# Kernel tuning notes

Hardware: AMD Instinct MI355X
Metric: run time of the kernel (lower is better)

## Reference

```python
import jax, jax.numpy as jnp
import numpy as np

DIM = 1024
HEADS = 16
HEAD_DIM = DIM // HEADS
THRESH = 0.29514
SHARP = 15.0
LN_EPS = 1e-5
NORM_EPS = 1e-12


def setup_inputs() -> dict:
    key = jax.random.key(0)
    ks = jax.random.split(key, 8)
    s = 1.0 / np.sqrt(DIM)
    sg = 1.0 / np.sqrt(HEAD_DIM)
    return {
        "x": jax.random.normal(ks[0], (2, 2048, DIM), dtype=jnp.float32),
        "Wq": jax.random.uniform(ks[1], (DIM, DIM), jnp.float32, -s, s),
        "Wk": jax.random.uniform(ks[2], (DIM, DIM), jnp.float32, -s, s),
        "Wv": jax.random.uniform(ks[3], (DIM, DIM), jnp.float32, -s, s),
        "gq": jax.random.uniform(ks[4], (HEAD_DIM,), jnp.float32, -sg, sg),
        "gk": jax.random.uniform(ks[5], (HEAD_DIM,), jnp.float32, -sg, sg),
        "Wo": jax.random.uniform(ks[6], (DIM, DIM), jnp.float32, -s, s),
        "bo": jax.random.uniform(ks[7], (DIM,), jnp.float32, -s, s),
        "ln_w": jnp.ones((DIM,), jnp.float32),
        "ln_b": jnp.zeros((DIM,), jnp.float32),
    }


def _l2norm(t):
    # F.normalize: t / max(||t||_2, eps)
    n = jnp.sqrt(jnp.sum(t * t, axis=-1, keepdims=True))
    return t / jnp.maximum(n, NORM_EPS)


def reference(x, Wq, Wk, Wv, gq, gk, Wo, bo, ln_w, ln_b):
    B, T, D = x.shape
    # LayerNorm over last dim
    mu = jnp.mean(x, axis=-1, keepdims=True)
    var = jnp.mean((x - mu) ** 2, axis=-1, keepdims=True)
    x_norm = (x - mu) / jnp.sqrt(var + LN_EPS) * ln_w + ln_b

    def split_heads(t):  # [B,T,D] -> [B,H,T,hd]
        return t.reshape(B, T, HEADS, HEAD_DIM).transpose(0, 2, 1, 3)

    q = _l2norm(split_heads(x_norm @ Wq))
    k = _l2norm(split_heads(x_norm @ Wk))
    v = split_heads(x @ Wv)  # note: v uses un-normalized x, as in source

    align = jnp.einsum("bhtd,bhsd->bhts", q, k)  # cosine alignment
    resonance = jax.nn.sigmoid((align - THRESH) * SHARP)
    gate_q = jnp.einsum("bhtd,d->bht", q, gq)
    gate_k = jnp.einsum("bhsd,d->bhs", k, gk)
    modulation = resonance * gate_q[..., :, None] * gate_k[..., None, :]
    collapse = jnp.einsum("bhts,bhsd->bhtd", modulation, v)
    collapse = collapse.transpose(0, 2, 1, 3).reshape(B, T, D)
    return collapse @ Wo + bo
```

## Files before the change

### kernel.cpp

```cpp
#include <hip/hip_runtime.h>
#include <math.h>

#define DIM 1024
#define T_SEQ 2048
#define NBATCH 2
#define HEADS 16
#define HD 64
#define NTOK 4096
#define THRESH 0.29514f
#define SHARP 15.0f
#define LOG2E 1.4426950408889634f

typedef __attribute__((ext_vector_type(8))) short bf16x8;
typedef __attribute__((ext_vector_type(4))) float f32x4;

__device__ __forceinline__ unsigned short f2b(float f) {
    unsigned int u = __float_as_uint(f);
    unsigned int r = (u + 0x7FFFu + ((u >> 16) & 1u)) >> 16;
    return (unsigned short)r;
}
__device__ __forceinline__ float b2f(unsigned short u) {
    return __uint_as_float(((unsigned int)u) << 16);
}

__device__ __forceinline__ void async_cp16(const unsigned short* g, unsigned short* l) {
    __builtin_amdgcn_global_load_lds(
        (const __attribute__((address_space(1))) unsigned int*)g,
        (__attribute__((address_space(3))) unsigned int*)l, 16, 0, 0);
}

__global__ __launch_bounds__(256) void ln_xnorm_kernel(
    const float* __restrict__ x, const float* __restrict__ lnw, const float* __restrict__ lnb,
    unsigned short* __restrict__ xnb, unsigned short* __restrict__ xb) {
    int row = blockIdx.x * 4 + (threadIdx.x >> 6);
    int lane = threadIdx.x & 63;
    const float4* xr = (const float4*)(x + (size_t)row * DIM);
    float4 v[4];
    float s = 0.f, ss = 0.f;
#pragma unroll
    for (int i = 0; i < 4; i++) {
        v[i] = xr[lane + i * 64];
        s += v[i].x + v[i].y + v[i].z + v[i].w;
        ss += v[i].x * v[i].x + v[i].y * v[i].y + v[i].z * v[i].z + v[i].w * v[i].w;
    }
#pragma unroll
    for (int off = 32; off; off >>= 1) {
        s += __shfl_xor(s, off);
        ss += __shfl_xor(ss, off);
    }
    float m = s * (1.f / DIM);
    float rstd = rsqrtf(ss * (1.f / DIM) - m * m + 1e-5f);
#pragma unroll
    for (int i = 0; i < 4; i++) {
        int e = (lane + i * 64) * 4;
        float4 lw = *(const float4*)&lnw[e];
        float4 lb = *(const float4*)&lnb[e];
        ushort4 un, ur;
        un.x = f2b((v[i].x - m) * rstd * lw.x + lb.x);
        un.y = f2b((v[i].y - m) * rstd * lw.y + lb.y);
        un.z = f2b((v[i].z - m) * rstd * lw.z + lb.z);
        un.w = f2b((v[i].w - m) * rstd * lw.w + lb.w);
        ur.x = f2b(v[i].x); ur.y = f2b(v[i].y); ur.z = f2b(v[i].z); ur.w = f2b(v[i].w);
        *(ushort4*)&xnb[(size_t)row * DIM + e] = un;
        *(ushort4*)&xb[(size_t)row * DIM + e] = ur;
    }
}

__global__ __launch_bounds__(256) void wtrans_kernel(
    const float* __restrict__ W0, const float* __restrict__ W1,
    const float* __restrict__ W2, const float* __restrict__ W3,
    unsigned short* __restrict__ T0, unsigned short* __restrict__ T1,
    unsigned short* __restrict__ T2, unsigned short* __restrict__ T3) {
    __shared__ float tile[64][65];
    const int z = blockIdx.z;
    const float* W = (z == 0) ? W0 : (z == 1) ? W1 : (z == 2) ? W2 : W3;
    unsigned short* T = (z == 0) ? T0 : (z == 1) ? T1 : (z == 2) ? T2 : T3;
    const int k0 = blockIdx.x * 64, n0 = blockIdx.y * 64;
    const int r = threadIdx.x >> 3;
    const int c = (threadIdx.x & 7) * 8;
#pragma unroll
    for (int half = 0; half < 2; half++) {
        int rr = r + half * 32;
        float4 a = *(const float4*)&W[(size_t)(k0 + rr) * DIM + n0 + c];
        float4 b = *(const float4*)&W[(size_t)(k0 + rr) * DIM + n0 + c + 4];
        tile[rr][c + 0] = a.x; tile[rr][c + 1] = a.y; tile[rr][c + 2] = a.z; tile[rr][c + 3] = a.w;
        tile[rr][c + 4] = b.x; tile[rr][c + 5] = b.y; tile[rr][c + 6] = b.z; tile[rr][c + 7] = b.w;
    }
    __syncthreads();
#pragma unroll
    for (int half = 0; half < 2; half++) {
        int dd = r + half * 32;
        bf16x8 o;
#pragma unroll
        for (int j = 0; j < 8; j++) o[j] = (short)f2b(tile[c + j][dd]);
        *(bf16x8*)&T[(size_t)(n0 + dd) * DIM + k0 + c] = o;
    }
}

template <int MODE>
__global__ __launch_bounds__(256) void gemm_mfma_kernel(
    const unsigned short* __restrict__ A0, const unsigned short* __restrict__ A2,
    const unsigned short* __restrict__ Bt0, const unsigned short* __restrict__ Bt1,
    const unsigned short* __restrict__ Bt2, const float* __restrict__ bias,
    const float* __restrict__ gq, const float* __restrict__ gk,
    unsigned short* __restrict__ Oq, unsigned short* __restrict__ Ok,
    unsigned short* __restrict__ Ov, float* __restrict__ gq_t, float* __restrict__ gk_t,
    float* __restrict__ Oout) {
    __shared__ __align__(16) unsigned short As[128 * 32];
    __shared__ __align__(16) unsigned short Bs[128 * 32];
    const int tid = threadIdx.x;
    const int lane = tid & 63, w = tid >> 6;
    const int l16 = lane & 15, quad = lane >> 4;
    const int wm = w >> 1, wn = w & 1;
    const int m0 = blockIdx.x * 128, n0 = blockIdx.y * 128;
    const unsigned short* A;
    const unsigned short* Bt;
    int z = 0;
    if constexpr (MODE == 0) {
        z = blockIdx.z;
        A = (z == 2) ? A2 : A0;
        Bt = (z == 0) ? Bt0 : (z == 1) ? Bt1 : Bt2;
    } else {
        A = A0;
        Bt = Bt0;
    }
    f32x4 acc[4][4] = {};
    const int kswz = (l16 >> 1) & 3;

    for (int k0 = 0; k0 < DIM; k0 += 32) {
        __syncthreads();
#pragma unroll
        for (int i = 0; i < 2; i++) {
            int linear = i * 256 + tid;
            int m = linear >> 2, kgp = linear & 3;
            int kgl = kgp ^ ((m >> 1) & 3);
            async_cp16(A + (size_t)(m0 + m) * DIM + k0 + kgl * 8, As + linear * 8);
            async_cp16(Bt + (size_t)(n0 + m) * DIM + k0 + kgl * 8, Bs + linear * 8);
        }
        __syncthreads();
        bf16x8 af[4], bfr[4];
#pragma unroll
        for (int t = 0; t < 4; t++) {
            int ma = wm * 64 + t * 16 + l16;
            af[t] = *(const bf16x8*)(As + ma * 32 + ((quad ^ kswz) * 8));
            int nb = wn * 64 + t * 16 + l16;
            bfr[t] = *(const bf16x8*)(Bs + nb * 32 + ((quad ^ kswz) * 8));
        }
#pragma unroll
        for (int mt = 0; mt < 4; mt++)
#pragma unroll
            for (int nt = 0; nt < 4; nt++)
                acc[mt][nt] =
                    __builtin_amdgcn_mfma_f32_16x16x32_bf16(af[mt], bfr[nt], acc[mt][nt], 0, 0, 0);
    }

    if constexpr (MODE == 0) {
        const int h = (n0 + wn * 64) >> 6;
        if (z <= 1) {
            const float* gvec = (z == 0) ? gq : gk;
            float* gate = (z == 0) ? gq_t : gk_t;
            unsigned short* O = (z == 0) ? Oq : Ok;
            float gv[4];
#pragma unroll
            for (int nt = 0; nt < 4; nt++) gv[nt] = gvec[nt * 16 + l16];
#pragma unroll
            for (int mt = 0; mt < 4; mt++) {
#pragma unroll
                for (int r = 0; r < 4; r++) {
                    float ss = 0.f;
#pragma unroll
                    for (int nt = 0; nt < 4; nt++) ss += acc[mt][nt][r] * acc[mt][nt][r];
#pragma unroll
                    for (int msk = 1; msk < 16; msk <<= 1) ss += __shfl_xor(ss, msk);
                    float rn = __builtin_amdgcn_rcpf(fmaxf(sqrtf(ss), 1e-12f));
                    float vn[4], gg = 0.f;
#pragma unroll
                    for (int nt = 0; nt < 4; nt++) {
                        vn[nt] = acc[mt][nt][r] * rn;
                        gg += vn[nt] * gv[nt];
                    }
#pragma unroll
                    for (int msk = 1; msk < 16; msk <<= 1) gg += __shfl_xor(gg, msk);
                    int tok = m0 + wm * 64 + mt * 16 + quad * 4 + r;
                    int b = tok >> 11, t = tok & 2047;
                    size_t rowbase = ((size_t)(b * HEADS + h) * T_SEQ + t) * HD;
#pragma unroll
                    for (int nt = 0; nt < 4; nt++) O[rowbase + nt * 16 + l16] = f2b(vn[nt]);
                    if (l16 == 0) gate[(b * HEADS + h) * T_SEQ + t] = gg;
                }
            }
        } else {
#pragma unroll
            for (int mt = 0; mt < 4; mt++) {
#pragma unroll
                for (int r = 0; r < 4; r++) {
                    int tok = m0 + wm * 64 + mt * 16 + quad * 4 + r;
                    int b = tok >> 11, t = tok & 2047;
                    size_t rowbase = ((size_t)(b * HEADS + h) * T_SEQ + t) * HD;
#pragma unroll
                    for (int nt = 0; nt < 4; nt++)
                        Ov[rowbase + nt * 16 + l16] = f2b(acc[mt][nt][r]);
                }
            }
        }
    } else {
        float bias_r[4];
#pragma unroll
        for (int nt = 0; nt < 4; nt++) bias_r[nt] = bias[n0 + wn * 64 + nt * 16 + l16];
#pragma unroll
        for (int mt = 0; mt < 4; mt++) {
#pragma unroll
            for (int r = 0; r < 4; r++) {
                int tok = m0 + wm * 64 + mt * 16 + quad * 4 + r;
#pragma unroll
                for (int nt = 0; nt < 4; nt++) {
                    int n = n0 + wn * 64 + nt * 16 + l16;
                    Oout[(size_t)tok * DIM + n] = acc[mt][nt][r] + bias_r[nt];
                }
            }
        }
    }
}

__global__ __launch_bounds__(256) void vtrans_kernel(const unsigned short* __restrict__ Vn,
                                                     const float* __restrict__ gk_t,
                                                     unsigned short* __restrict__ Vt) {
    __shared__ float tile[64][65];
    const int bh = blockIdx.y;
    const int t0 = blockIdx.x * 64;
    const int r = threadIdx.x >> 3;
    const int c = (threadIdx.x & 7) * 8;
    const unsigned short* src = Vn + (size_t)bh * T_SEQ * HD;
#pragma unroll
    for (int half = 0; half < 2; half++) {
        int rr = r + half * 32;
        float gkv = gk_t[bh * T_SEQ + t0 + rr];
        bf16x8 v = *(const bf16x8*)(src + (size_t)(t0 + rr) * HD + c);
#pragma unroll
        for (int j = 0; j < 8; j++) tile[rr][c + j] = b2f((unsigned short)v[j]) * gkv;
    }
    __syncthreads();
    unsigned short* dst = Vt + (size_t)bh * HD * T_SEQ;
#pragma unroll
    for (int half = 0; half < 2; half++) {
        int dd = r + half * 32;
        bf16x8 o;
#pragma unroll
        for (int j = 0; j < 8; j++) o[j] = (short)f2b(tile[c + j][dd]);
        *(bf16x8*)(dst + (size_t)dd * T_SEQ + t0 + c) = o;
    }
}

__global__ __launch_bounds__(256) void attn_mfma_kernel(
    const unsigned short* __restrict__ Qn, const unsigned short* __restrict__ Kn,
    const unsigned short* __restrict__ Vt, const float* __restrict__ gateq,
    unsigned short* __restrict__ collb) {
    __shared__ __align__(16) unsigned short Ks[64 * 72];
    __shared__ __align__(16) unsigned short VtL[64 * 72];
    __shared__ __align__(16) unsigned short Sw[4 * 16 * 72];
    const int tid = threadIdx.x;
    const int lane = tid & 63, w = tid >> 6;
    const int quad = lane >> 4, l16 = lane & 15;
    const int t0 = blockIdx.x * 64;
    const int h = blockIdx.y, b = blockIdx.z;
    const int bh = b * HEADS + h;
    const size_t base = (size_t)bh * T_SEQ * HD;
    constexpr float K1 = -SHARP * LOG2E;
    constexpr float K0 = THRESH * SHARP * LOG2E;

    const unsigned short* qrow = Qn + base + (size_t)(t0 + w * 16 + l16) * HD;
    bf16x8 fq0 = *(const bf16x8*)(qrow + quad * 8);
    bf16x8 fq1 = *(const bf16x8*)(qrow + 32 + quad * 8);

    f32x4 oacc[4] = {};
    unsigned short* myS = &Sw[w * 16 * 72];
    const int sr = tid >> 3;
    const int sc = (tid & 7) * 8;

    for (int s0 = 0; s0 < T_SEQ; s0 += 64) {
        __syncthreads();
#pragma unroll
        for (int half = 0; half < 2; half++) {
            int rr = sr + half * 32;
            bf16x8 kv = *(const bf16x8*)(Kn + base + (size_t)(s0 + rr) * HD + sc);
            *(bf16x8*)(Ks + rr * 72 + sc) = kv;
            bf16x8 vv = *(const bf16x8*)(Vt + base + (size_t)rr * T_SEQ + s0 + sc);
            *(bf16x8*)(VtL + rr * 72 + sc) = vv;
        }
        __syncthreads();

#pragma unroll
        for (int ct = 0; ct < 4; ct++) {
            f32x4 sacc = {0.f, 0.f, 0.f, 0.f};
            bf16x8 fk0 = *(const bf16x8*)(Ks + (ct * 16 + l16) * 72 + quad * 8);
            bf16x8 fk1 = *(const bf16x8*)(Ks + (ct * 16 + l16) * 72 + 32 + quad * 8);
            sacc = __builtin_amdgcn_mfma_f32_16x16x32_bf16(fq0, fk0, sacc, 0, 0, 0);
            sacc = __builtin_amdgcn_mfma_f32_16x16x32_bf16(fq1, fk1, sacc, 0, 0, 0);
#pragma unroll
            for (int r = 0; r < 4; r++) {
                float e = __builtin_amdgcn_exp2f(fmaf(sacc[r], K1, K0));
                float wv = __builtin_amdgcn_rcpf(1.f + e);
                myS[(quad * 4 + r) * 72 + ct * 16 + l16] = f2b(wv);
            }
        }
        __syncthreads();

        bf16x8 fs0 = *(const bf16x8*)(myS + l16 * 72 + quad * 8);
        bf16x8 fs1 = *(const bf16x8*)(myS + l16 * 72 + 32 + quad * 8);
#pragma unroll
        for (int dt = 0; dt < 4; dt++) {
            bf16x8 fv0 = *(const bf16x8*)(VtL + (dt * 16 + l16) * 72 + quad * 8);
            bf16x8 fv1 = *(const bf16x8*)(VtL + (dt * 16 + l16) * 72 + 32 + quad * 8);
            oacc[dt] = __builtin_amdgcn_mfma_f32_16x16x32_bf16(fs0, fv0, oacc[dt], 0, 0, 0);
            oacc[dt] = __builtin_amdgcn_mfma_f32_16x16x32_bf16(fs1, fv1, oacc[dt], 0, 0, 0);
        }
    }

#pragma unroll
    for (int r = 0; r < 4; r++) {
        int t = t0 + w * 16 + quad * 4 + r;
        float gq_v = gateq[bh * T_SEQ + t];
        unsigned short* dst = collb + ((size_t)b * T_SEQ + t) * DIM + h * HD;
#pragma unroll
        for (int dt = 0; dt < 4; dt++) dst[dt * 16 + l16] = f2b(oacc[dt][r] * gq_v);
    }
}

extern "C" void kernel_launch(void* const* d_in, const int* in_sizes, int n_in,
                              void* d_out, int out_size, void* d_ws, size_t ws_size,
                              hipStream_t stream) {
    const float* x = (const float*)d_in[0];
    const float* Wq = (const float*)d_in[1];
    const float* Wk = (const float*)d_in[2];
    const float* Wv = (const float*)d_in[3];
    const float* gq = (const float*)d_in[4];
    const float* gk = (const float*)d_in[5];
    const float* Wo = (const float*)d_in[6];
    const float* bo = (const float*)d_in[7];
    const float* lnw = (const float*)d_in[8];
    const float* lnb = (const float*)d_in[9];
    float* out = (float*)d_out;

    unsigned short* ws = (unsigned short*)d_ws;
    unsigned short* xnb = ws;
    unsigned short* xb = xnb + (size_t)NTOK * DIM;
    unsigned short* Wqt = xb + (size_t)NTOK * DIM;
    unsigned short* Wkt = Wqt + (size_t)DIM * DIM;
    unsigned short* Wvt = Wkt + (size_t)DIM * DIM;
    unsigned short* Wot = Wvt + (size_t)DIM * DIM;
    unsigned short* Q16 = Wot + (size_t)DIM * DIM;
    unsigned short* K16 = Q16 + (size_t)NTOK * DIM;
    unsigned short* Vn = K16 + (size_t)NTOK * DIM;
    float* gq_t = (float*)(Vn + (size_t)NTOK * DIM);
    float* gk_t = gq_t + NBATCH * HEADS * T_SEQ;
    unsigned short* Vt = xnb;
    unsigned short* collb = xb;

    ln_xnorm_kernel<<<NTOK / 4, 256, 0, stream>>>(x, lnw, lnb, xnb, xb);
    wtrans_kernel<<<dim3(16, 16, 4), 256, 0, stream>>>(Wq, Wk, Wv, Wo, Wqt, Wkt, Wvt, Wot);
    gemm_mfma_kernel<0><<<dim3(NTOK / 128, DIM / 128, 3), 256, 0, stream>>>(
        xnb, xb, Wqt, Wkt, Wvt, nullptr, gq, gk, Q16, K16, Vn, gq_t, gk_t, nullptr);
    vtrans_kernel<<<dim3(T_SEQ / 64, NBATCH * HEADS), 256, 0, stream>>>(Vn, gk_t, Vt);
    attn_mfma_kernel<<<dim3(T_SEQ / 64, HEADS, NBATCH), 256, 0, stream>>>(
        Q16, K16, Vt, gq_t, collb);
    gemm_mfma_kernel<1><<<dim3(NTOK / 128, DIM / 128, 1), 256, 0, stream>>>(
        collb, nullptr, Wot, nullptr, nullptr, bo, nullptr, nullptr, nullptr, nullptr, nullptr,
        nullptr, nullptr, out);
}
```

Before: 250.8 us.

## Double-buffer K/V tiles and double query rows per block in attention

The attention kernel now processes 128 query rows per block (32 per wave), so each K/V tile loaded into shared memory is reused twice as much. K/V loads for the next tile are prefetched into registers and stored into a second LDS buffer, which removes one barrier per iteration and overlaps global loads with MFMA work. MFMA operands are swapped so score and output tiles come out transposed, which allows vectorized ushort4 writes to LDS and to global output. The cost is more registers and LDS per block and half as many blocks in the grid (512), which may reduce occupancy.

```diff
diff --git a/kernel.cpp b/kernel.cpp
--- a/kernel.cpp
+++ b/kernel.cpp
@@ -255,74 +255,110 @@
     const unsigned short* __restrict__ Qn, const unsigned short* __restrict__ Kn,
     const unsigned short* __restrict__ Vt, const float* __restrict__ gateq,
     unsigned short* __restrict__ collb) {
-    __shared__ __align__(16) unsigned short Ks[64 * 72];
-    __shared__ __align__(16) unsigned short VtL[64 * 72];
-    __shared__ __align__(16) unsigned short Sw[4 * 16 * 72];
+    __shared__ __align__(16) unsigned short Ks[2][64 * 72];
+    __shared__ __align__(16) unsigned short VtL[2][64 * 72];
+    __shared__ __align__(16) unsigned short Sw[4][32 * 72];
     const int tid = threadIdx.x;
     const int lane = tid & 63, w = tid >> 6;
     const int quad = lane >> 4, l16 = lane & 15;
-    const int t0 = blockIdx.x * 64;
+    const int t0 = blockIdx.x * 128;
     const int h = blockIdx.y, b = blockIdx.z;
     const int bh = b * HEADS + h;
     const size_t base = (size_t)bh * T_SEQ * HD;
     constexpr float K1 = -SHARP * LOG2E;
     constexpr float K0 = THRESH * SHARP * LOG2E;
 
-    const unsigned short* qrow = Qn + base + (size_t)(t0 + w * 16 + l16) * HD;
-    bf16x8 fq0 = *(const bf16x8*)(qrow + quad * 8);
-    bf16x8 fq1 = *(const bf16x8*)(qrow + 32 + quad * 8);
-
-    f32x4 oacc[4] = {};
-    unsigned short* myS = &Sw[w * 16 * 72];
+    bf16x8 fq[2][2];
+#pragma unroll
+    for (int mt = 0; mt < 2; mt++) {
+        const unsigned short* qrow = Qn + base + (size_t)(t0 + w * 32 + mt * 16 + l16) * HD;
+        fq[mt][0] = *(const bf16x8*)(qrow + quad * 8);
+        fq[mt][1] = *(const bf16x8*)(qrow + 32 + quad * 8);
+    }
+
+    f32x4 oacc[4][2] = {};
+    unsigned short* myS = Sw[w];
     const int sr = tid >> 3;
     const int sc = (tid & 7) * 8;
 
-    for (int s0 = 0; s0 < T_SEQ; s0 += 64) {
+    bf16x8 kr0, kr1, vr0, vr1;
+    kr0 = *(const bf16x8*)(Kn + base + (size_t)sr * HD + sc);
+    kr1 = *(const bf16x8*)(Kn + base + (size_t)(sr + 32) * HD + sc);
+    vr0 = *(const bf16x8*)(Vt + base + (size_t)sr * T_SEQ + sc);
+    vr1 = *(const bf16x8*)(Vt + base + (size_t)(sr + 32) * T_SEQ + sc);
+    *(bf16x8*)(Ks[0] + sr * 72 + sc) = kr0;
+    *(bf16x8*)(Ks[0] + (sr + 32) * 72 + sc) = kr1;
+    *(bf16x8*)(VtL[0] + sr * 72 + sc) = vr0;
+    *(bf16x8*)(VtL[0] + (sr + 32) * 72 + sc) = vr1;
+    __syncthreads();
+
+    for (int i = 0; i < T_SEQ / 64; i++) {
+        const unsigned short* ksb = Ks[i & 1];
+        const unsigned short* vtb = VtL[i & 1];
+        const bool more = (i + 1) < (T_SEQ / 64);
+        if (more) {
+            int s0n = (i + 1) * 64;
+            kr0 = *(const bf16x8*)(Kn + base + (size_t)(s0n + sr) * HD + sc);
+            kr1 = *(const bf16x8*)(Kn + base + (size_t)(s0n + sr + 32) * HD + sc);
+            vr0 = *(const bf16x8*)(Vt + base + (size_t)sr * T_SEQ + s0n + sc);
+            vr1 = *(const bf16x8*)(Vt + base + (size_t)(sr + 32) * T_SEQ + s0n + sc);
+        }
+
+#pragma unroll
+        for (int ct = 0; ct < 4; ct++) {
+            bf16x8 fk0 = *(const bf16x8*)(ksb + (ct * 16 + l16) * 72 + quad * 8);
+            bf16x8 fk1 = *(const bf16x8*)(ksb + (ct * 16 + l16) * 72 + 32 + quad * 8);
+#pragma unroll
+            for (int mt = 0; mt < 2; mt++) {
+                f32x4 sacc = {0.f, 0.f, 0.f, 0.f};
+                sacc = __builtin_amdgcn_mfma_f32_16x16x32_bf16(fk0, fq[mt][0], sacc, 0, 0, 0);
+                sacc = __builtin_amdgcn_mfma_f32_16x16x32_bf16(fk1, fq[mt][1], sacc, 0, 0, 0);
+                ushort4 p;
+                p.x = f2b(__builtin_amdgcn_rcpf(1.f + __builtin_amdgcn_exp2f(fmaf(sacc[0], K1, K0))));
+                p.y = f2b(__builtin_amdgcn_rcpf(1.f + __builtin_amdgcn_exp2f(fmaf(sacc[1], K1, K0))));
+                p.z = f2b(__builtin_amdgcn_rcpf(1.f + __builtin_amdgcn_exp2f(fmaf(sacc[2], K1, K0))));
+                p.w = f2b(__builtin_amdgcn_rcpf(1.f + __builtin_amdgcn_exp2f(fmaf(sacc[3], K1, K0))));
+                *(ushort4*)(myS + (mt * 16 + l16) * 72 + ct * 16 + quad * 4) = p;
+            }
+        }
+
+#pragma unroll
+        for (int kh = 0; kh < 2; kh++) {
+            bf16x8 fs0 = *(const bf16x8*)(myS + (0 * 16 + l16) * 72 + kh * 32 + quad * 8);
+            bf16x8 fs1 = *(const bf16x8*)(myS + (1 * 16 + l16) * 72 + kh * 32 + quad * 8);
+#pragma unroll
+            for (int dt = 0; dt < 4; dt++) {
+                bf16x8 fv = *(const bf16x8*)(vtb + (dt * 16 + l16) * 72 + kh * 32 + quad * 8);
+                oacc[dt][0] = __builtin_amdgcn_mfma_f32_16x16x32_bf16(fv, fs0, oacc[dt][0], 0, 0, 0);
+                oacc[dt][1] = __builtin_amdgcn_mfma_f32_16x16x32_bf16(fv, fs1, oacc[dt][1], 0, 0, 0);
+            }
+        }
+
+        if (more) {
+            unsigned short* ksn = Ks[(i + 1) & 1];
+            unsigned short* vtn = VtL[(i + 1) & 1];
+            *(bf16x8*)(ksn + sr * 72 + sc) = kr0;
+            *(bf16x8*)(ksn + (sr + 32) * 72 + sc) = kr1;
+            *(bf16x8*)(vtn + sr * 72 + sc) = vr0;
+            *(bf16x8*)(vtn + (sr + 32) * 72 + sc) = vr1;
+        }
         __syncthreads();
-#pragma unroll
-        for (int half = 0; half < 2; half++) {
-            int rr = sr + half * 32;
-            bf16x8 kv = *(const bf16x8*)(Kn + base + (size_t)(s0 + rr) * HD + sc);
-            *(bf16x8*)(Ks + rr * 72 + sc) = kv;
-            bf16x8 vv = *(const bf16x8*)(Vt + base + (size_t)rr * T_SEQ + s0 + sc);
-            *(bf16x8*)(VtL + rr * 72 + sc) = vv;
-        }
-        __syncthreads();
-
-#pragma unroll
-        for (int ct = 0; ct < 4; ct++) {
-            f32x4 sacc = {0.f, 0.f, 0.f, 0.f};
-            bf16x8 fk0 = *(const bf16x8*)(Ks + (ct * 16 + l16) * 72 + quad * 8);
-            bf16x8 fk1 = *(const bf16x8*)(Ks + (ct * 16 + l16) * 72 + 32 + quad * 8);
-            sacc = __builtin_amdgcn_mfma_f32_16x16x32_bf16(fq0, fk0, sacc, 0, 0, 0);
-            sacc = __builtin_amdgcn_mfma_f32_16x16x32_bf16(fq1, fk1, sacc, 0, 0, 0);
-#pragma unroll
-            for (int r = 0; r < 4; r++) {
-                float e = __builtin_amdgcn_exp2f(fmaf(sacc[r], K1, K0));
-                float wv = __builtin_amdgcn_rcpf(1.f + e);
-                myS[(quad * 4 + r) * 72 + ct * 16 + l16] = f2b(wv);
-            }
-        }
-        __syncthreads();
-
-        bf16x8 fs0 = *(const bf16x8*)(myS + l16 * 72 + quad * 8);
-        bf16x8 fs1 = *(const bf16x8*)(myS + l16 * 72 + 32 + quad * 8);
-#pragma unroll
-        for (int dt = 0; dt < 4; dt++) {
-            bf16x8 fv0 = *(const bf16x8*)(VtL + (dt * 16 + l16) * 72 + quad * 8);
-            bf16x8 fv1 = *(const bf16x8*)(VtL + (dt * 16 + l16) * 72 + 32 + quad * 8);
-            oacc[dt] = __builtin_amdgcn_mfma_f32_16x16x32_bf16(fs0, fv0, oacc[dt], 0, 0, 0);
-            oacc[dt] = __builtin_amdgcn_mfma_f32_16x16x32_bf16(fs1, fv1, oacc[dt], 0, 0, 0);
-        }
-    }
-
-#pragma unroll
-    for (int r = 0; r < 4; r++) {
-        int t = t0 + w * 16 + quad * 4 + r;
+    }
+
+#pragma unroll
+    for (int mt = 0; mt < 2; mt++) {
+        int t = t0 + w * 32 + mt * 16 + l16;
         float gq_v = gateq[bh * T_SEQ + t];
         unsigned short* dst = collb + ((size_t)b * T_SEQ + t) * DIM + h * HD;
 #pragma unroll
-        for (int dt = 0; dt < 4; dt++) dst[dt * 16 + l16] = f2b(oacc[dt][r] * gq_v);
+        for (int dt = 0; dt < 4; dt++) {
+            ushort4 o;
+            o.x = f2b(oacc[dt][mt][0] * gq_v);
+            o.y = f2b(oacc[dt][mt][1] * gq_v);
+            o.z = f2b(oacc[dt][mt][2] * gq_v);
+            o.w = f2b(oacc[dt][mt][3] * gq_v);
+            *(ushort4*)(dst + dt * 16 + quad * 4) = o;
+        }
     }
 }
 
@@ -361,7 +397,7 @@
     gemm_mfma_kernel<0><<<dim3(NTOK / 128, DIM / 128, 3), 256, 0, stream>>>(
         xnb, xb, Wqt, Wkt, Wvt, nullptr, gq, gk, Q16, K16, Vn, gq_t, gk_t, nullptr);
     vtrans_kernel<<<dim3(T_SEQ / 64, NBATCH * HEADS), 256, 0, stream>>>(Vn, gk_t, Vt);
-    attn_mfma_kernel<<<dim3(T_SEQ / 64, HEADS, NBATCH), 256, 0, stream>>>(
+    attn_mfma_kernel<<<dim3(T_SEQ / 128, HEADS, NBATCH), 256, 0, stream>>>(
         Q16, K16, Vt, gq_t, collb);
     gemm_mfma_kernel<1><<<dim3(NTOK / 128, DIM / 128, 1), 256, 0, stream>>>(
         collb, nullptr, Wot, nullptr, nullptr, bo, nullptr, nullptr, nullptr, nullptr, nullptr,
```

Result: faster. 236.6 us (-5.7%).
